# Optimization experiments

Measured on AMD Instinct MI355X. Metric: run time of the kernel, lower is better.

Reference implementation:

```python
import jax, jax.numpy as jnp
import numpy as np

B, N, E, H, DEPTH = 2, 2048, 1024, 8, 12
D = E // H // 2  # head_dim = 64
LN_EPS = 1e-5


def setup_inputs() -> dict:
    key = jax.random.key(0)
    ks = jax.random.split(key, 10)
    w = lambda k: jax.random.normal(k, (E, E), jnp.float32) * (E ** -0.5)
    lp = lambda k: jax.random.normal(k, (D,), jnp.float32) * 0.1
    return {
        "x": jax.random.normal(ks[0], (B, N, E), jnp.float32),
        "Wq": w(ks[1]), "Wk": w(ks[2]), "Wv": w(ks[3]), "Wo": w(ks[4]),
        "lq1": lp(ks[5]), "lk1": lp(ks[6]), "lq2": lp(ks[7]), "lk2": lp(ks[8]),
        "ln_g": jnp.ones((2 * D,), jnp.float32),
        "ln_b": jnp.zeros((2 * D,), jnp.float32),
    }


def reference(x, Wq, Wk, Wv, Wo, lq1, lk1, lq2, lk2, ln_g, ln_b):
    b, n, e = x.shape
    lam_init = 0.8 - 0.6 * np.exp(-0.3 * DEPTH)  # lambda_init_fn(depth)
    # projections; split into 2H half-heads of dim D for q,k; H heads of dim 2D for v
    q = (x @ Wq).reshape(b, n, 2 * H, D).transpose(0, 2, 1, 3) * (D ** -0.5)  # [b,2H,n,D]
    k = (x @ Wk).reshape(b, n, 2 * H, D).transpose(0, 2, 1, 3)                # [b,2H,n,D]
    v = (x @ Wv).reshape(b, n, H, 2 * D).transpose(0, 2, 1, 3)                # [b,H,n,2D]
    scores = jnp.einsum('bhqd,bhkd->bhqk', q, k)                              # [b,2H,n,n]
    attn = jax.nn.softmax(scores, axis=-1).reshape(b, H, 2, n, n)
    lam = jnp.exp(jnp.sum(lq1 * lk1)) - jnp.exp(jnp.sum(lq2 * lk2)) + lam_init
    w_diff = attn[:, :, 0] - lam * attn[:, :, 1]                              # [b,H,n,n]
    o = jnp.einsum('bhqk,bhkd->bhqd', w_diff, v)                              # [b,H,n,2D]
    # per-head LayerNorm over channel dim 2D
    mu = o.mean(-1, keepdims=True)
    var = ((o - mu) ** 2).mean(-1, keepdims=True)
    o = (o - mu) * jax.lax.rsqrt(var + LN_EPS) * ln_g + ln_b
    o = o.transpose(0, 2, 1, 3).reshape(b, n, e)
    return o @ Wo
```

## Files before the change

### kernel.cpp

```cpp
#include <hip/hip_runtime.h>
#include <hip/hip_bf16.h>
#include <math.h>

#define B_ 2
#define N_ 2048
#define E_ 1024
#define H_ 8

typedef __attribute__((ext_vector_type(8))) short frag8;
typedef __attribute__((ext_vector_type(4))) float f32x4;
typedef __attribute__((ext_vector_type(16))) float f32x16;
typedef __attribute__((ext_vector_type(8))) unsigned short u16x8;

constexpr float LAM_INIT = 0.7836057665316245f;
constexpr float LOG2E = 1.4426950408889634f;
constexpr float EXP2_GUARD = -23.083120654f;

static __device__ __forceinline__ float fast_exp2(float x) {
#if __has_builtin(__builtin_amdgcn_exp2f)
  return __builtin_amdgcn_exp2f(x);
#else
  return exp2f(x);
#endif
}

static __device__ __forceinline__ ushort f2bf(float f) {
  union { float f; unsigned u; } v; v.f = f;
  unsigned r = (v.u + 0x7FFFu + ((v.u >> 16) & 1u)) >> 16;
  return (ushort)r;
}

static __device__ __forceinline__ unsigned pkbf(float a, float b) {
  __hip_bfloat162 h = __float22bfloat162_rn(make_float2(a, b));
  return *(unsigned*)&h;
}

static __device__ __forceinline__ float bf2f_lo(unsigned u) {
  union { unsigned u; float f; } v; v.u = u << 16; return v.f;
}
static __device__ __forceinline__ float bf2f_hi(unsigned u) {
  union { unsigned u; float f; } v; v.u = u & 0xFFFF0000u; return v.f;
}

static __device__ __forceinline__ void async16(const void* g, void* l) {
  __builtin_amdgcn_global_load_lds((const __attribute__((address_space(1))) void*)g,
                                   (__attribute__((address_space(3))) void*)l, 16, 0, 0);
}

__global__ __launch_bounds__(256) void prep_kernel(
    const float* __restrict__ x,
    const float* __restrict__ Wq, const float* __restrict__ Wk,
    const float* __restrict__ Wv, const float* __restrict__ Wo,
    const float* __restrict__ lq1, const float* __restrict__ lk1,
    const float* __restrict__ lq2, const float* __restrict__ lk2,
    ushort* __restrict__ xb, ushort* __restrict__ wqkvt, ushort* __restrict__ wot,
    float* __restrict__ lam_out) {
  __shared__ ushort t[64][72];
  const int bx = blockIdx.x;
  const int tid = threadIdx.x;
  if (bx < 2048) {
    int i = bx * 256 + tid;
    const float4* sp = (const float4*)x + (size_t)i * 2;
    float4 a = sp[0], b = sp[1];
    u16x8 o;
    o[0] = f2bf(a.x); o[1] = f2bf(a.y); o[2] = f2bf(a.z); o[3] = f2bf(a.w);
    o[4] = f2bf(b.x); o[5] = f2bf(b.y); o[6] = f2bf(b.z); o[7] = f2bf(b.w);
    *(u16x8*)(xb + (size_t)i * 8) = o;
  } else if (bx < 3072) {
    int idx = bx - 2048;
    int sel = idx >> 8, rem = idx & 255;
    const float* W = (sel == 0) ? Wq : (sel == 1) ? Wk : (sel == 2) ? Wv : Wo;
    ushort* Wt = (sel < 3) ? (wqkvt + (size_t)sel * 1048576) : wot;
    const int c0 = (rem & 15) * 64, r0 = (rem >> 4) * 64;
    {
      int r = tid >> 2, cc = (tid & 3) * 16;
      const float* sp = W + (size_t)(r0 + r) * 1024 + c0 + cc;
      #pragma unroll
      for (int j = 0; j < 4; j++) {
        float4 a = *(const float4*)(sp + j * 4);
        t[cc + j * 4 + 0][r] = f2bf(a.x);
        t[cc + j * 4 + 1][r] = f2bf(a.y);
        t[cc + j * 4 + 2][r] = f2bf(a.z);
        t[cc + j * 4 + 3][r] = f2bf(a.w);
      }
    }
    __syncthreads();
    int c = tid >> 2, rr = (tid & 3) * 16;
    ushort* dp = Wt + (size_t)(c0 + c) * 1024 + r0 + rr;
    *(u16x8*)dp = *(u16x8*)&t[c][rr];
    *(u16x8*)(dp + 8) = *(u16x8*)&t[c][rr + 8];
  } else {
    if (tid < 64) {
      float t1 = lq1[tid] * lk1[tid];
      float t2 = lq2[tid] * lk2[tid];
      #pragma unroll
      for (int off = 32; off > 0; off >>= 1) {
        t1 += __shfl_down(t1, off);
        t2 += __shfl_down(t2, off);
      }
      if (tid == 0) lam_out[0] = expf(t1) - expf(t2) + LAM_INIT;
    }
  }
}

__global__ __launch_bounds__(256) void gemm_qkv(const ushort* __restrict__ xb,
                                                const ushort* __restrict__ wqkvt,
                                                ushort* __restrict__ qkb,
                                                ushort* __restrict__ vtb, float qscale) {
  __shared__ ushort As[4096];
  __shared__ ushort Bs[4096];
  const int id = blockIdx.x;
  const ushort* A; const ushort* Bt; ushort* C;
  int m0, n0, ldc;
  float sc;
  if (id < 512) {
    m0 = (id >> 4) * 128; n0 = (id & 15) * 128;
    A = xb; Bt = wqkvt; C = qkb; ldc = 2048;
    sc = (n0 < 1024) ? qscale : 1.0f;
  } else {
    int id2 = id - 512;
    m0 = (id2 & 7) * 128; n0 = (id2 >> 3) * 128;
    A = wqkvt + 2 * 1048576; Bt = xb; C = vtb; ldc = 4096;
    sc = 1.0f;
  }
  const int tid = threadIdx.x;
  const int w = tid >> 6, l = tid & 63;
  const int quad = l >> 4, col16 = l & 15;
  const int wm = (w & 1) * 64, wn = (w >> 1) * 64;
  const int lrow = l >> 2, lcol = (l & 3) * 8;

  f32x4 acc[4][4];
  #pragma unroll
  for (int mt = 0; mt < 4; mt++)
    #pragma unroll
    for (int nt = 0; nt < 4; nt++) acc[mt][nt] = (f32x4){0.f, 0.f, 0.f, 0.f};

  for (int k0 = 0; k0 < 1024; k0 += 32) {
    __syncthreads();
    #pragma unroll
    for (int i = 0; i < 4; i++) {
      int s = w * 4 + i;
      if (s < 8) {
        const ushort* gp = A + (size_t)(m0 + s * 16 + lrow) * 1024 + k0 + lcol;
        async16(gp, (char*)As + s * 1024);
      } else {
        int s2 = s - 8;
        const ushort* gp = Bt + (size_t)(n0 + s2 * 16 + lrow) * 1024 + k0 + lcol;
        async16(gp, (char*)Bs + s2 * 1024);
      }
    }
    __syncthreads();
    frag8 af[4], bfr[4];
    #pragma unroll
    for (int mt = 0; mt < 4; mt++)
      af[mt] = *(const frag8*)((const char*)As + (wm + mt * 16 + col16) * 64 + quad * 16);
    #pragma unroll
    for (int nt = 0; nt < 4; nt++)
      bfr[nt] = *(const frag8*)((const char*)Bs + (wn + nt * 16 + col16) * 64 + quad * 16);
    #pragma unroll
    for (int mt = 0; mt < 4; mt++)
      #pragma unroll
      for (int nt = 0; nt < 4; nt++)
        acc[mt][nt] = __builtin_amdgcn_mfma_f32_16x16x32_bf16(af[mt], bfr[nt], acc[mt][nt], 0, 0, 0);
  }

  #pragma unroll
  for (int mt = 0; mt < 4; mt++)
    #pragma unroll
    for (int r = 0; r < 4; r++) {
      int m = m0 + wm + mt * 16 + quad * 4 + r;
      #pragma unroll
      for (int nt = 0; nt < 4; nt++) {
        int n = n0 + wn + nt * 16 + col16;
        C[(size_t)m * ldc + n] = f2bf(acc[mt][nt][r] * sc);
      }
    }
}

__global__ __launch_bounds__(256) void gemm_out(const ushort* __restrict__ A,
                                                const ushort* __restrict__ Bt,
                                                float* __restrict__ Cp) {
  __shared__ ushort As[2048];
  __shared__ ushort Bs[4096];
  const int tid = threadIdx.x;
  const int w = tid >> 6, l = tid & 63;
  const int quad = l >> 4, col16 = l & 15;
  const int m0 = blockIdx.y * 64, n0 = blockIdx.x * 128;
  const int wm = (w & 1) * 32, wn = (w >> 1) * 64;
  const int lrow = l >> 2, lcol = (l & 3) * 8;

  f32x4 acc[2][4];
  #pragma unroll
  for (int mt = 0; mt < 2; mt++)
    #pragma unroll
    for (int nt = 0; nt < 4; nt++) acc[mt][nt] = (f32x4){0.f, 0.f, 0.f, 0.f};

  for (int k0 = 0; k0 < 1024; k0 += 32) {
    __syncthreads();
    #pragma unroll
    for (int i = 0; i < 3; i++) {
      int s = w * 3 + i;
      if (s < 4) {
        const ushort* gp = A + (size_t)(m0 + s * 16 + lrow) * 1024 + k0 + lcol;
        async16(gp, (char*)As + s * 1024);
      } else {
        int s2 = s - 4;
        const ushort* gp = Bt + (size_t)(n0 + s2 * 16 + lrow) * 1024 + k0 + lcol;
        async16(gp, (char*)Bs + s2 * 1024);
      }
    }
    __syncthreads();
    frag8 af[2], bfr[4];
    #pragma unroll
    for (int mt = 0; mt < 2; mt++)
      af[mt] = *(const frag8*)((const char*)As + (wm + mt * 16 + col16) * 64 + quad * 16);
    #pragma unroll
    for (int nt = 0; nt < 4; nt++)
      bfr[nt] = *(const frag8*)((const char*)Bs + (wn + nt * 16 + col16) * 64 + quad * 16);
    #pragma unroll
    for (int mt = 0; mt < 2; mt++)
      #pragma unroll
      for (int nt = 0; nt < 4; nt++)
        acc[mt][nt] = __builtin_amdgcn_mfma_f32_16x16x32_bf16(af[mt], bfr[nt], acc[mt][nt], 0, 0, 0);
  }

  #pragma unroll
  for (int mt = 0; mt < 2; mt++)
    #pragma unroll
    for (int r = 0; r < 4; r++) {
      int m = m0 + wm + mt * 16 + quad * 4 + r;
      #pragma unroll
      for (int nt = 0; nt < 4; nt++) {
        int n = n0 + wn + nt * 16 + col16;
        Cp[(size_t)m * 1024 + n] = acc[mt][nt][r];
      }
    }
}

__global__ __launch_bounds__(256, 2) void flash_kernel(const ushort* __restrict__ qk,
                                                       const ushort* __restrict__ vt,
                                                       ushort* __restrict__ opart,
                                                       float* __restrict__ lbuf) {
  const int h2 = blockIdx.y;
  const int b = blockIdx.z >> 1, ks = blockIdx.z & 1;
  const int h = h2 >> 1;
  const int tid = threadIdx.x;
  const int w = tid >> 6;
  const int lane31 = tid & 31, half = (tid & 63) >> 5;
  const int i0 = blockIdx.x * 128 + w * 32;

  __shared__ ushort Klds0[64 * 64], Klds1[64 * 64];
  __shared__ ushort Vlds0[128 * 64], Vlds1[128 * 64];

  frag8 qf[4];
  #pragma unroll
  for (int chk = 0; chk < 4; chk++) {
    const ushort* qp = qk + (size_t)(b * N_ + i0 + lane31) * 2048 +
                       h2 * 64 + chk * 16 + half * 8;
    qf[chk] = *(const frag8*)qp;
  }

  f32x16 o_[4];
  #pragma unroll
  for (int cm = 0; cm < 4; cm++)
    #pragma unroll
    for (int i = 0; i < 16; i++) o_[cm][i] = 0.f;
  float la0 = 0.f, la1 = 0.f;

  auto stage = [&](int k0, ushort* Kb, ushort* Vb) {
    #pragma unroll
    for (int it = 0; it < 2; it++) {
      int j = it * 256 + tid;
      int row = j >> 3, sch = (j & 7) ^ (row & 7);
      const ushort* kg = qk + (size_t)(b * N_ + k0 + row) * 2048 + 1024 + h2 * 64 + sch * 8;
      async16(kg, (char*)Kb + it * 4096 + w * 1024);
    }
    #pragma unroll
    for (int it = 0; it < 4; it++) {
      int j = it * 256 + tid;
      int row = j >> 3, sch = (j & 7) ^ (row & 7);
      const ushort* vg = vt + (size_t)(h * 128 + row) * 4096 + b * N_ + k0 + sch * 8;
      async16(vg, (char*)Vb + it * 4096 + w * 1024);
    }
  };

  auto compute = [&](const ushort* Kb, const ushort* Vb) {
    #pragma unroll
    for (int kh = 0; kh < 2; kh++) {
      f32x16 st;
      #pragma unroll
      for (int i = 0; i < 16; i++) st[i] = EXP2_GUARD;
      const int r = kh * 32 + lane31;
      #pragma unroll
      for (int chk = 0; chk < 4; chk++) {
        frag8 a = *(const frag8*)((const char*)Kb + r * 128 +
                                  (((chk << 1) | half) ^ (r & 7)) * 16);
        st = __builtin_amdgcn_mfma_f32_32x32x16_bf16(a, qf[chk], st, 0, 0, 0);
      }
      unsigned pk[8];
      #pragma unroll
      for (int p = 0; p < 8; p++) {
        float e0 = fast_exp2(st[2 * p]);
        float e1 = fast_exp2(st[2 * p + 1]);
        la0 += e0;
        la1 += e1;
        pk[p] = pkbf(e0, e1);
      }
      #pragma unroll
      for (int c16 = 0; c16 < 2; c16++) {
        unsigned p0 = pk[c16 * 4 + 0], p1 = pk[c16 * 4 + 1];
        unsigned p2 = pk[c16 * 4 + 2], p3 = pk[c16 * 4 + 3];
        unsigned m1 = (unsigned)__shfl_xor((int)(half ? p0 : p2), 32);
        unsigned m2 = (unsigned)__shfl_xor((int)(half ? p1 : p3), 32);
        union { unsigned u[4]; frag8 f; } u;
        u.u[0] = half ? m1 : p0;
        u.u[1] = half ? m2 : p1;
        u.u[2] = half ? p2 : m1;
        u.u[3] = half ? p3 : m2;
        frag8 bfr = u.f;
        #pragma unroll
        for (int cm = 0; cm < 4; cm++) {
          int c = cm * 32 + lane31;
          int g = (kh * 4 + c16 * 2 + half) ^ (c & 7);
          frag8 a = *(const frag8*)((const char*)Vb + c * 128 + g * 16);
          o_[cm] = __builtin_amdgcn_mfma_f32_32x32x16_bf16(a, bfr, o_[cm], 0, 0, 0);
        }
      }
    }
  };

  const int kbeg = ks * 1024;
  stage(kbeg, Klds0, Vlds0);
  #pragma unroll 1
  for (int kt2 = 0; kt2 < 8; kt2++) {
    const int k0 = kbeg + kt2 * 128;
    __syncthreads();
    stage(k0 + 64, Klds1, Vlds1);
    compute(Klds0, Vlds0);
    __syncthreads();
    if (kt2 < 7)
      stage(k0 + 128, Klds0, Vlds0);
    compute(Klds1, Vlds1);
  }

  float l_acc = la0 + la1;
  float lt = l_acc + __shfl_xor(l_acc, 32);
  if (half == 0)
    lbuf[(size_t)ks * 65536 + (size_t)(b * 16 + h2) * N_ + i0 + lane31] = lt;

  ushort* obase = opart + (size_t)ks * 8388608;
  {
    int q = i0 + lane31;
    ushort* ob = obase + ((size_t)((b * 16 + h2) * N_ + q)) * 128;
    #pragma unroll
    for (int cm = 0; cm < 4; cm++)
      #pragma unroll
      for (int g = 0; g < 4; g++) {
        int c = cm * 32 + g * 8 + half * 4;
        uint2 pv;
        pv.x = pkbf(o_[cm][4 * g + 0], o_[cm][4 * g + 1]);
        pv.y = pkbf(o_[cm][4 * g + 2], o_[cm][4 * g + 3]);
        *(uint2*)(ob + c) = pv;
      }
  }
}

__global__ __launch_bounds__(256) void combine_ln_kernel(
    const ushort* __restrict__ opart, const float* __restrict__ lbuf,
    const float* __restrict__ lam_p,
    const float* __restrict__ ln_g, const float* __restrict__ ln_b,
    ushort* __restrict__ onorm) {
  const float lam = lam_p[0];
  const int wave = threadIdx.x >> 6, lane = threadIdx.x & 63;
  const int row = blockIdx.x * 4 + wave;
  const int n = row & (N_ - 1);
  const int bh = row >> 11;
  const int h = bh & (H_ - 1);
  const int b = bh >> 3;

  const size_t re = (size_t)(b * 16 + 2 * h) * N_ + n;
  const size_t ro = (size_t)(b * 16 + 2 * h + 1) * N_ + n;
  const float rle = 1.0f / (lbuf[re] + lbuf[65536 + re]);
  const float rlo = 1.0f / (lbuf[ro] + lbuf[65536 + ro]);

  const int c = lane * 2;
  unsigned e0 = *(const unsigned*)(opart + re * 128 + c);
  unsigned e1 = *(const unsigned*)(opart + 8388608 + re * 128 + c);
  unsigned q0 = *(const unsigned*)(opart + ro * 128 + c);
  unsigned q1 = *(const unsigned*)(opart + 8388608 + ro * 128 + c);
  float ve0 = (bf2f_lo(e0) + bf2f_lo(e1)) * rle;
  float ve1 = (bf2f_hi(e0) + bf2f_hi(e1)) * rle;
  float vo0 = (bf2f_lo(q0) + bf2f_lo(q1)) * rlo;
  float vo1 = (bf2f_hi(q0) + bf2f_hi(q1)) * rlo;
  float v0 = ve0 - lam * vo0;
  float v1 = ve1 - lam * vo1;
  float sum = v0 + v1, ss = v0 * v0 + v1 * v1;
  #pragma unroll
  for (int off = 1; off < 64; off <<= 1) {
    sum += __shfl_xor(sum, off);
    ss += __shfl_xor(ss, off);
  }
  float mu = sum * (1.0f / 128.0f);
  float var = ss * (1.0f / 128.0f) - mu * mu;
  float r = rsqrtf(var + 1e-5f);
  float o0 = (v0 - mu) * r * ln_g[c] + ln_b[c];
  float o1 = (v1 - mu) * r * ln_g[c + 1] + ln_b[c + 1];
  unsigned pkv = (unsigned)f2bf(o0) | ((unsigned)f2bf(o1) << 16);
  *(unsigned*)(onorm + ((size_t)(b * N_ + n)) * E_ + h * 128 + c) = pkv;
}

extern "C" void kernel_launch(void* const* d_in, const int* in_sizes, int n_in,
                              void* d_out, int out_size, void* d_ws, size_t ws_size,
                              hipStream_t stream) {
  const float* x    = (const float*)d_in[0];
  const float* Wq   = (const float*)d_in[1];
  const float* Wk   = (const float*)d_in[2];
  const float* Wv   = (const float*)d_in[3];
  const float* Wo   = (const float*)d_in[4];
  const float* lq1  = (const float*)d_in[5];
  const float* lk1  = (const float*)d_in[6];
  const float* lq2  = (const float*)d_in[7];
  const float* lk2  = (const float*)d_in[8];
  const float* ln_g = (const float*)d_in[9];
  const float* ln_b = (const float*)d_in[10];
  float* out = (float*)d_out;

  const size_t MN = (size_t)B_ * N_ * E_;
  ushort* xb    = (ushort*)d_ws;
  ushort* wqkvt = xb + MN;
  ushort* wot   = wqkvt + 3 * 1048576;
  ushort* qkb   = wot + 1048576;
  ushort* vtb   = qkb + (size_t)4096 * 2048;
  ushort* op    = vtb + MN;
  float*  lbuf  = (float*)(op + 4 * MN);
  float*  lam   = lbuf + 2 * 65536;
  ushort* onorm = xb;

  prep_kernel<<<dim3(3073), 256, 0, stream>>>(x, Wq, Wk, Wv, Wo, lq1, lk1, lq2, lk2,
                                              xb, wqkvt, wot, lam);

  gemm_qkv<<<dim3(768), 256, 0, stream>>>(xb, wqkvt, qkb, vtb, 0.125f * LOG2E);

  flash_kernel<<<dim3(N_ / 128, 16, B_ * 2), 256, 0, stream>>>(qkb, vtb, op, lbuf);
  combine_ln_kernel<<<dim3(B_ * H_ * N_ / 4), 256, 0, stream>>>(op, lbuf, lam, ln_g, ln_b, onorm);
  gemm_out<<<dim3(8, 64), 256, 0, stream>>>(onorm, wot, out);
}
```

Baseline: 228.4 us.

## Process two query tiles per wave in flash kernel and use permlane32 swap

Each wave now handles 64 query rows (two 32-row tiles) instead of 32, so every K and V fragment read from LDS feeds two MFMAs. This halves LDS traffic and staging per query and doubles the block's query span. The cross-half shuffle that builds the P fragment is replaced by the permlane32_swap builtin. The cost is roughly double the accumulator registers, which risks spills or lower occupancy, and half as many blocks (512), which may underfill the GPU.

```diff
diff --git a/kernel.cpp b/kernel.cpp
--- a/kernel.cpp
+++ b/kernel.cpp
@@ -45,6 +45,18 @@
 static __device__ __forceinline__ void async16(const void* g, void* l) {
   __builtin_amdgcn_global_load_lds((const __attribute__((address_space(1))) void*)g,
                                    (__attribute__((address_space(3))) void*)l, 16, 0, 0);
+}
+
+static __device__ __forceinline__ frag8 mkfrag(unsigned p0, unsigned p1,
+                                               unsigned p2, unsigned p3) {
+  auto r02 = __builtin_amdgcn_permlane32_swap((int)p0, (int)p2, false, false);
+  auto r13 = __builtin_amdgcn_permlane32_swap((int)p1, (int)p3, false, false);
+  union { unsigned u[4]; frag8 f; } u;
+  u.u[0] = (unsigned)r02[0];
+  u.u[1] = (unsigned)r13[0];
+  u.u[2] = (unsigned)r02[1];
+  u.u[3] = (unsigned)r13[1];
+  return u.f;
 }
 
 __global__ __launch_bounds__(256) void prep_kernel(
@@ -247,25 +259,28 @@
   const int tid = threadIdx.x;
   const int w = tid >> 6;
   const int lane31 = tid & 31, half = (tid & 63) >> 5;
-  const int i0 = blockIdx.x * 128 + w * 32;
+  const int i0 = blockIdx.x * 256 + w * 64;
 
   __shared__ ushort Klds0[64 * 64], Klds1[64 * 64];
   __shared__ ushort Vlds0[128 * 64], Vlds1[128 * 64];
 
-  frag8 qf[4];
+  frag8 qf0[4], qf1[4];
   #pragma unroll
   for (int chk = 0; chk < 4; chk++) {
-    const ushort* qp = qk + (size_t)(b * N_ + i0 + lane31) * 2048 +
-                       h2 * 64 + chk * 16 + half * 8;
-    qf[chk] = *(const frag8*)qp;
-  }
-
-  f32x16 o_[4];
+    const ushort* qp0 = qk + (size_t)(b * N_ + i0 + lane31) * 2048 +
+                        h2 * 64 + chk * 16 + half * 8;
+    qf0[chk] = *(const frag8*)qp0;
+    const ushort* qp1 = qk + (size_t)(b * N_ + i0 + 32 + lane31) * 2048 +
+                        h2 * 64 + chk * 16 + half * 8;
+    qf1[chk] = *(const frag8*)qp1;
+  }
+
+  f32x16 o0_[4], o1_[4];
   #pragma unroll
   for (int cm = 0; cm < 4; cm++)
     #pragma unroll
-    for (int i = 0; i < 16; i++) o_[cm][i] = 0.f;
-  float la0 = 0.f, la1 = 0.f;
+    for (int i = 0; i < 16; i++) { o0_[cm][i] = 0.f; o1_[cm][i] = 0.f; }
+  float la00 = 0.f, la01 = 0.f, la10 = 0.f, la11 = 0.f;
 
   auto stage = [&](int k0, ushort* Kb, ushort* Vb) {
     #pragma unroll
@@ -287,43 +302,44 @@
   auto compute = [&](const ushort* Kb, const ushort* Vb) {
     #pragma unroll
     for (int kh = 0; kh < 2; kh++) {
-      f32x16 st;
-      #pragma unroll
-      for (int i = 0; i < 16; i++) st[i] = EXP2_GUARD;
+      f32x16 st0, st1;
+      #pragma unroll
+      for (int i = 0; i < 16; i++) { st0[i] = EXP2_GUARD; st1[i] = EXP2_GUARD; }
       const int r = kh * 32 + lane31;
       #pragma unroll
       for (int chk = 0; chk < 4; chk++) {
         frag8 a = *(const frag8*)((const char*)Kb + r * 128 +
                                   (((chk << 1) | half) ^ (r & 7)) * 16);
-        st = __builtin_amdgcn_mfma_f32_32x32x16_bf16(a, qf[chk], st, 0, 0, 0);
-      }
-      unsigned pk[8];
+        st0 = __builtin_amdgcn_mfma_f32_32x32x16_bf16(a, qf0[chk], st0, 0, 0, 0);
+        st1 = __builtin_amdgcn_mfma_f32_32x32x16_bf16(a, qf1[chk], st1, 0, 0, 0);
+      }
+      unsigned pk0[8], pk1[8];
       #pragma unroll
       for (int p = 0; p < 8; p++) {
-        float e0 = fast_exp2(st[2 * p]);
-        float e1 = fast_exp2(st[2 * p + 1]);
-        la0 += e0;
-        la1 += e1;
-        pk[p] = pkbf(e0, e1);
+        float e0 = fast_exp2(st0[2 * p]);
+        float e1 = fast_exp2(st0[2 * p + 1]);
+        la00 += e0;
+        la01 += e1;
+        pk0[p] = pkbf(e0, e1);
+        float f0 = fast_exp2(st1[2 * p]);
+        float f1 = fast_exp2(st1[2 * p + 1]);
+        la10 += f0;
+        la11 += f1;
+        pk1[p] = pkbf(f0, f1);
       }
       #pragma unroll
       for (int c16 = 0; c16 < 2; c16++) {
-        unsigned p0 = pk[c16 * 4 + 0], p1 = pk[c16 * 4 + 1];
-        unsigned p2 = pk[c16 * 4 + 2], p3 = pk[c16 * 4 + 3];
-        unsigned m1 = (unsigned)__shfl_xor((int)(half ? p0 : p2), 32);
-        unsigned m2 = (unsigned)__shfl_xor((int)(half ? p1 : p3), 32);
-        union { unsigned u[4]; frag8 f; } u;
-        u.u[0] = half ? m1 : p0;
-        u.u[1] = half ? m2 : p1;
-        u.u[2] = half ? p2 : m1;
-        u.u[3] = half ? p3 : m2;
-        frag8 bfr = u.f;
+        frag8 b0 = mkfrag(pk0[c16 * 4 + 0], pk0[c16 * 4 + 1],
+                          pk0[c16 * 4 + 2], pk0[c16 * 4 + 3]);
+        frag8 b1 = mkfrag(pk1[c16 * 4 + 0], pk1[c16 * 4 + 1],
+                          pk1[c16 * 4 + 2], pk1[c16 * 4 + 3]);
         #pragma unroll
         for (int cm = 0; cm < 4; cm++) {
           int c = cm * 32 + lane31;
           int g = (kh * 4 + c16 * 2 + half) ^ (c & 7);
           frag8 a = *(const frag8*)((const char*)Vb + c * 128 + g * 16);
-          o_[cm] = __builtin_amdgcn_mfma_f32_32x32x16_bf16(a, bfr, o_[cm], 0, 0, 0);
+          o0_[cm] = __builtin_amdgcn_mfma_f32_32x32x16_bf16(a, b0, o0_[cm], 0, 0, 0);
+          o1_[cm] = __builtin_amdgcn_mfma_f32_32x32x16_bf16(a, b1, o1_[cm], 0, 0, 0);
         }
       }
     }
@@ -343,10 +359,14 @@
     compute(Klds1, Vlds1);
   }
 
-  float l_acc = la0 + la1;
-  float lt = l_acc + __shfl_xor(l_acc, 32);
-  if (half == 0)
-    lbuf[(size_t)ks * 65536 + (size_t)(b * 16 + h2) * N_ + i0 + lane31] = lt;
+  float l0 = la00 + la01;
+  l0 += __shfl_xor(l0, 32);
+  float l1 = la10 + la11;
+  l1 += __shfl_xor(l1, 32);
+  if (half == 0) {
+    lbuf[(size_t)ks * 65536 + (size_t)(b * 16 + h2) * N_ + i0 + lane31] = l0;
+    lbuf[(size_t)ks * 65536 + (size_t)(b * 16 + h2) * N_ + i0 + 32 + lane31] = l1;
+  }
 
   ushort* obase = opart + (size_t)ks * 8388608;
   {
@@ -358,8 +378,22 @@
       for (int g = 0; g < 4; g++) {
         int c = cm * 32 + g * 8 + half * 4;
         uint2 pv;
-        pv.x = pkbf(o_[cm][4 * g + 0], o_[cm][4 * g + 1]);
-        pv.y = pkbf(o_[cm][4 * g + 2], o_[cm][4 * g + 3]);
+        pv.x = pkbf(o0_[cm][4 * g + 0], o0_[cm][4 * g + 1]);
+        pv.y = pkbf(o0_[cm][4 * g + 2], o0_[cm][4 * g + 3]);
+        *(uint2*)(ob + c) = pv;
+      }
+  }
+  {
+    int q = i0 + 32 + lane31;
+    ushort* ob = obase + ((size_t)((b * 16 + h2) * N_ + q)) * 128;
+    #pragma unroll
+    for (int cm = 0; cm < 4; cm++)
+      #pragma unroll
+      for (int g = 0; g < 4; g++) {
+        int c = cm * 32 + g * 8 + half * 4;
+        uint2 pv;
+        pv.x = pkbf(o1_[cm][4 * g + 0], o1_[cm][4 * g + 1]);
+        pv.y = pkbf(o1_[cm][4 * g + 2], o1_[cm][4 * g + 3]);
         *(uint2*)(ob + c) = pv;
       }
   }
@@ -441,7 +475,7 @@
 
   gemm_qkv<<<dim3(768), 256, 0, stream>>>(xb, wqkvt, qkb, vtb, 0.125f * LOG2E);
 
-  flash_kernel<<<dim3(N_ / 128, 16, B_ * 2), 256, 0, stream>>>(qkb, vtb, op, lbuf);
+  flash_kernel<<<dim3(N_ / 256, 16, B_ * 2), 256, 0, stream>>>(qkb, vtb, op, lbuf);
   combine_ln_kernel<<<dim3(B_ * H_ * N_ / 4), 256, 0, stream>>>(op, lbuf, lam, ln_g, ln_b, onorm);
   gemm_out<<<dim3(8, 64), 256, 0, stream>>>(onorm, wot, out);
 }
```

After: 262.4 us. +14.9%, slower.

## Drop split-K in flash kernel and build P fragments with permlane32_swap

Applied to the files above, without the earlier changes.

Each flash block now walks the full key range instead of half of it. This removes the second partial output and l buffers and the extra reads and adds in the combine kernel. The grid halves from 1024 to 512 blocks, which may leave the GPU's compute units less evenly loaded. The cross-half exchange that assembles the P operand now uses two permlane32_swap intrinsics in place of shfl_xor plus selects, cutting the instruction count in the inner loop.

```diff
diff --git a/kernel.cpp b/kernel.cpp
--- a/kernel.cpp
+++ b/kernel.cpp
@@ -45,6 +45,18 @@
 static __device__ __forceinline__ void async16(const void* g, void* l) {
   __builtin_amdgcn_global_load_lds((const __attribute__((address_space(1))) void*)g,
                                    (__attribute__((address_space(3))) void*)l, 16, 0, 0);
+}
+
+static __device__ __forceinline__ frag8 mkfrag(unsigned p0, unsigned p1,
+                                               unsigned p2, unsigned p3) {
+  auto r02 = __builtin_amdgcn_permlane32_swap((int)p0, (int)p2, false, false);
+  auto r13 = __builtin_amdgcn_permlane32_swap((int)p1, (int)p3, false, false);
+  union { unsigned u[4]; frag8 f; } u;
+  u.u[0] = (unsigned)r02[0];
+  u.u[1] = (unsigned)r13[0];
+  u.u[2] = (unsigned)r02[1];
+  u.u[3] = (unsigned)r13[1];
+  return u.f;
 }
 
 __global__ __launch_bounds__(256) void prep_kernel(
@@ -242,7 +254,7 @@
                                                        ushort* __restrict__ opart,
                                                        float* __restrict__ lbuf) {
   const int h2 = blockIdx.y;
-  const int b = blockIdx.z >> 1, ks = blockIdx.z & 1;
+  const int b = blockIdx.z;
   const int h = h2 >> 1;
   const int tid = threadIdx.x;
   const int w = tid >> 6;
@@ -308,16 +320,8 @@
       }
       #pragma unroll
       for (int c16 = 0; c16 < 2; c16++) {
-        unsigned p0 = pk[c16 * 4 + 0], p1 = pk[c16 * 4 + 1];
-        unsigned p2 = pk[c16 * 4 + 2], p3 = pk[c16 * 4 + 3];
-        unsigned m1 = (unsigned)__shfl_xor((int)(half ? p0 : p2), 32);
-        unsigned m2 = (unsigned)__shfl_xor((int)(half ? p1 : p3), 32);
-        union { unsigned u[4]; frag8 f; } u;
-        u.u[0] = half ? m1 : p0;
-        u.u[1] = half ? m2 : p1;
-        u.u[2] = half ? p2 : m1;
-        u.u[3] = half ? p3 : m2;
-        frag8 bfr = u.f;
+        frag8 bfr = mkfrag(pk[c16 * 4 + 0], pk[c16 * 4 + 1],
+                           pk[c16 * 4 + 2], pk[c16 * 4 + 3]);
         #pragma unroll
         for (int cm = 0; cm < 4; cm++) {
           int c = cm * 32 + lane31;
@@ -329,16 +333,15 @@
     }
   };
 
-  const int kbeg = ks * 1024;
-  stage(kbeg, Klds0, Vlds0);
+  stage(0, Klds0, Vlds0);
   #pragma unroll 1
-  for (int kt2 = 0; kt2 < 8; kt2++) {
-    const int k0 = kbeg + kt2 * 128;
+  for (int kt2 = 0; kt2 < 16; kt2++) {
+    const int k0 = kt2 * 128;
     __syncthreads();
     stage(k0 + 64, Klds1, Vlds1);
     compute(Klds0, Vlds0);
     __syncthreads();
-    if (kt2 < 7)
+    if (kt2 < 15)
       stage(k0 + 128, Klds0, Vlds0);
     compute(Klds1, Vlds1);
   }
@@ -346,12 +349,11 @@
   float l_acc = la0 + la1;
   float lt = l_acc + __shfl_xor(l_acc, 32);
   if (half == 0)
-    lbuf[(size_t)ks * 65536 + (size_t)(b * 16 + h2) * N_ + i0 + lane31] = lt;
-
-  ushort* obase = opart + (size_t)ks * 8388608;
+    lbuf[(size_t)(b * 16 + h2) * N_ + i0 + lane31] = lt;
+
   {
     int q = i0 + lane31;
-    ushort* ob = obase + ((size_t)((b * 16 + h2) * N_ + q)) * 128;
+    ushort* ob = opart + ((size_t)((b * 16 + h2) * N_ + q)) * 128;
     #pragma unroll
     for (int cm = 0; cm < 4; cm++)
       #pragma unroll
@@ -380,18 +382,16 @@
 
   const size_t re = (size_t)(b * 16 + 2 * h) * N_ + n;
   const size_t ro = (size_t)(b * 16 + 2 * h + 1) * N_ + n;
-  const float rle = 1.0f / (lbuf[re] + lbuf[65536 + re]);
-  const float rlo = 1.0f / (lbuf[ro] + lbuf[65536 + ro]);
+  const float rle = 1.0f / lbuf[re];
+  const float rlo = 1.0f / lbuf[ro];
 
   const int c = lane * 2;
   unsigned e0 = *(const unsigned*)(opart + re * 128 + c);
-  unsigned e1 = *(const unsigned*)(opart + 8388608 + re * 128 + c);
   unsigned q0 = *(const unsigned*)(opart + ro * 128 + c);
-  unsigned q1 = *(const unsigned*)(opart + 8388608 + ro * 128 + c);
-  float ve0 = (bf2f_lo(e0) + bf2f_lo(e1)) * rle;
-  float ve1 = (bf2f_hi(e0) + bf2f_hi(e1)) * rle;
-  float vo0 = (bf2f_lo(q0) + bf2f_lo(q1)) * rlo;
-  float vo1 = (bf2f_hi(q0) + bf2f_hi(q1)) * rlo;
+  float ve0 = bf2f_lo(e0) * rle;
+  float ve1 = bf2f_hi(e0) * rle;
+  float vo0 = bf2f_lo(q0) * rlo;
+  float vo1 = bf2f_hi(q0) * rlo;
   float v0 = ve0 - lam * vo0;
   float v1 = ve1 - lam * vo1;
   float sum = v0 + v1, ss = v0 * v0 + v1 * v1;
@@ -432,8 +432,8 @@
   ushort* qkb   = wot + 1048576;
   ushort* vtb   = qkb + (size_t)4096 * 2048;
   ushort* op    = vtb + MN;
-  float*  lbuf  = (float*)(op + 4 * MN);
-  float*  lam   = lbuf + 2 * 65536;
+  float*  lbuf  = (float*)(op + 2 * MN);
+  float*  lam   = lbuf + 65536;
   ushort* onorm = xb;
 
   prep_kernel<<<dim3(3073), 256, 0, stream>>>(x, Wq, Wk, Wv, Wo, lq1, lk1, lq2, lk2,
@@ -441,7 +441,7 @@
 
   gemm_qkv<<<dim3(768), 256, 0, stream>>>(xb, wqkvt, qkb, vtb, 0.125f * LOG2E);
 
-  flash_kernel<<<dim3(N_ / 128, 16, B_ * 2), 256, 0, stream>>>(qkb, vtb, op, lbuf);
+  flash_kernel<<<dim3(N_ / 128, 16, B_), 256, 0, stream>>>(qkb, vtb, op, lbuf);
   combine_ln_kernel<<<dim3(B_ * H_ * N_ / 4), 256, 0, stream>>>(op, lbuf, lam, ln_g, ln_b, onorm);
   gemm_out<<<dim3(8, 64), 256, 0, stream>>>(onorm, wot, out);
 }
```

Result: faster. 219.7 us (-3.8%).
